# Kernel optimization log

Hardware: AMD Instinct MI355X
Metric: run time of the kernel (lower is better)

The kernel has to match this reference:

```python
import jax, jax.numpy as jnp
import numpy as np

N_NODES = 98304
N_GRAPHS = 2048
NODES_PER_GRAPH = 48
N_EDGES = 393216
NODE_IN = 128
EMB = 64
HID = 256
N_LAYERS = 6
ATTN_DIM = 256
N_HEADS = 4
HEAD_DIM = ATTN_DIM // N_HEADS
OUT_DIM = 1024


def setup_inputs() -> dict:
    key = jax.random.key(0)
    ks = iter(jax.random.split(key, 40))

    def nrm(shape, fan_in):
        return (jax.random.normal(next(ks), shape, dtype=jnp.float32)
                / np.float32(np.sqrt(fan_in)))

    x = jax.random.normal(next(ks), (N_NODES, NODE_IN), dtype=jnp.float32)
    edge_index = jax.random.randint(next(ks), (2, N_EDGES), 0, N_NODES, dtype=jnp.int32)
    batch = (jnp.arange(N_NODES, dtype=jnp.int32) // NODES_PER_GRAPH)

    inp = {
        "x": x,
        "edge_index": edge_index,
        "batch": batch,
        "W_embed": nrm((NODE_IN, EMB), NODE_IN),
        "b_embed": jnp.zeros((EMB,), jnp.float32),
        "W1": nrm((N_LAYERS, EMB, HID), EMB),
        "b1": jnp.zeros((N_LAYERS, HID), jnp.float32),
        "W2": nrm((N_LAYERS, HID, 2 * HID), HID),
        "b2": jnp.zeros((N_LAYERS, 2 * HID), jnp.float32),
        "W3": nrm((N_LAYERS, 2 * HID, EMB), 2 * HID),
        "b3": jnp.zeros((N_LAYERS, EMB), jnp.float32),
        "Wp": nrm((EMB, ATTN_DIM), EMB),
        "bp": jnp.zeros((ATTN_DIM,), jnp.float32),
        "q": jax.random.normal(next(ks), (1, ATTN_DIM), dtype=jnp.float32),
        "W_in": nrm((ATTN_DIM, 3 * ATTN_DIM), ATTN_DIM),
        "b_in": jnp.zeros((3 * ATTN_DIM,), jnp.float32),
        "W_out": nrm((ATTN_DIM, ATTN_DIM), ATTN_DIM),
        "b_out": jnp.zeros((ATTN_DIM,), jnp.float32),
        "Wh1": nrm((ATTN_DIM, HID), ATTN_DIM),
        "bh1": jnp.zeros((HID,), jnp.float32),
        "ln_g": jnp.ones((HID,), jnp.float32),
        "ln_b": jnp.zeros((HID,), jnp.float32),
        "Wh2": nrm((HID, OUT_DIM), HID),
        "bh2": jnp.zeros((OUT_DIM,), jnp.float32),
    }
    return inp


def _forward(x, edge_index, batch, W_embed, b_embed, W1, b1, W2, b2, W3, b3,
             Wp, bp, q, W_in, b_in, W_out, b_out, Wh1, bh1, ln_g, ln_b, Wh2, bh2):
    row = edge_index[0]  # only row is used, matching the torch module

    # node embed
    h = x @ W_embed + b_embed  # [N, 64]

    # 6 GNN layers: gather h[row] -> 3-layer MLP -> scatter_add back to row
    for l in range(N_LAYERS):
        m = jax.nn.relu(h[row] @ W1[l] + b1[l])          # [E, 256]
        m = jax.nn.relu(m @ W2[l] + b2[l])               # [E, 512]
        dh = m @ W3[l] + b3[l]                           # [E, 64]
        h = h + jax.ops.segment_sum(dh, row, num_segments=N_NODES)

    # attention pooling per graph (single learned query, 4 heads)
    hp = h @ Wp + bp                                     # [N, 256]
    Wq, Wk, Wv = W_in[:, :ATTN_DIM], W_in[:, ATTN_DIM:2 * ATTN_DIM], W_in[:, 2 * ATTN_DIM:]
    bq, bk, bv = b_in[:ATTN_DIM], b_in[ATTN_DIM:2 * ATTN_DIM], b_in[2 * ATTN_DIM:]

    qh = ((q @ Wq + bq).reshape(N_HEADS, HEAD_DIM)
          / jnp.asarray(np.sqrt(HEAD_DIM), jnp.float32))  # [H, D]
    k = (hp @ Wk + bk).reshape(N_NODES, N_HEADS, HEAD_DIM)
    v = (hp @ Wv + bv).reshape(N_NODES, N_HEADS, HEAD_DIM)

    scores = jnp.einsum('nhd,hd->nh', k, qh)             # [N, H]
    smax = jax.ops.segment_max(scores, batch, num_segments=N_GRAPHS)  # [B, H]
    e = jnp.exp(scores - smax[batch])
    denom = jax.ops.segment_sum(e, batch, num_segments=N_GRAPHS)      # [B, H]
    w = e / denom[batch]                                  # [N, H]
    pooled = jax.ops.segment_sum(w[:, :, None] * v, batch, num_segments=N_GRAPHS)  # [B, H, D]
    attn = pooled.reshape(N_GRAPHS, ATTN_DIM) @ W_out + b_out  # [B, 256]

    # projection head: ReLU -> Linear -> ReLU -> LayerNorm -> Linear
    t = jax.nn.relu(attn) @ Wh1 + bh1
    t = jax.nn.relu(t)
    mu = jnp.mean(t, axis=-1, keepdims=True)
    var = jnp.mean((t - mu) ** 2, axis=-1, keepdims=True)
    t = (t - mu) * jax.lax.rsqrt(var + 1e-5) * ln_g + ln_b
    return t @ Wh2 + bh2                                  # [B, 1024]


def reference(x, edge_index, batch, W_embed, b_embed, W1, b1, W2, b2, W3, b3,
              Wp, bp, q, W_in, b_in, W_out, b_out, Wh1, bh1, ln_g, ln_b, Wh2, bh2):
    return _forward(x, edge_index, batch, W_embed, b_embed, W1, b1, W2, b2, W3, b3,
                    Wp, bp, q, W_in, b_in, W_out, b_out, Wh1, bh1, ln_g, ln_b, Wh2, bh2)
```

## Files before the change

kernel.cpp:

```cpp
#include <hip/hip_runtime.h>
#include <hip/hip_bf16.h>

#define N_NODES 98304
#define N_GRAPHS 2048
#define N_EDGES 393216
#define EMB 64
#define HID 256
#define N_LAYERS_ 6

typedef __attribute__((ext_vector_type(8))) short short8v;
typedef __attribute__((ext_vector_type(4))) float f32x4;
#define MFMA16(a, b, c) __builtin_amdgcn_mfma_f32_16x16x32_bf16(a, b, c, 0, 0, 0)

__device__ __forceinline__ unsigned short f2bf(float x) {
    unsigned int u = __float_as_uint(x);
    u = (u + 0x7fffu + ((u >> 16) & 1u)) >> 16;
    return (unsigned short)u;
}
__device__ __forceinline__ float bf2f(unsigned short h) {
    return __uint_as_float(((unsigned int)h) << 16);
}
__device__ __forceinline__ int swz(int row, int col, int rowc) {
    return (row * rowc + col) ^ ((row & 7) << 3);
}

__global__ __launch_bounds__(256) void zero_cnt_kernel(int* __restrict__ cnt) {
    int i = blockIdx.x * 256 + threadIdx.x;
    if (i < N_NODES) cnt[i] = 0;
}
__global__ __launch_bounds__(256) void hist_kernel(const int* __restrict__ row,
                                                   int* __restrict__ cnt) {
    int i = blockIdx.x * 256 + threadIdx.x;
    if (i < N_EDGES) atomicAdd(&cnt[row[i]], 1);
}

__global__ __launch_bounds__(64) void prep_frag_kernel(
    const float* __restrict__ W, unsigned short* __restrict__ oh,
    unsigned short* __restrict__ ol, int K, int N)
{
    const int NF = N >> 4, KS = K >> 5;
    const int fpl = NF * KS;
    const int layer = blockIdx.x / fpl;
    const int fid = blockIdx.x % fpl;
    const int nf = fid / KS, ks = fid % KS;
    const int lane = threadIdx.x;
    const float* Wl = W + (size_t)layer * K * N;
    const int n = nf * 16 + (lane & 15);
    const int kb = ks * 32 + (lane >> 4) * 8;
    short8v vh, vl;
    #pragma unroll
    for (int j = 0; j < 8; j++) {
        float wv = Wl[(size_t)(kb + j) * N + n];
        unsigned short hi = f2bf(wv);
        vh[j] = (short)hi;
        vl[j] = (short)f2bf(wv - bf2f(hi));
    }
    size_t o = (size_t)layer * K * N + ((size_t)(nf * KS + ks) * 64 + lane) * 8;
    *reinterpret_cast<short8v*>(oh + o) = vh;
    *reinterpret_cast<short8v*>(ol + o) = vl;
}

__global__ __launch_bounds__(256) void gbuild_kernel(
    const float* __restrict__ Wp, const float* __restrict__ bp,
    const float* __restrict__ W_in, const float* __restrict__ b_in,
    float* __restrict__ Gm, float* __restrict__ Gd)
{
    const int idx = blockIdx.x * 256 + threadIdx.x;
    const int q = idx >> 8, p = idx & 255;
    float s = 0.f;
    if ((q >> 6) == (p >> 6)) {
        const float* wr = Wp + (q & 63) * 256;
        for (int j = 0; j < 256; j++) s += wr[j] * W_in[j * 768 + 512 + p];
    }
    Gm[q * 256 + p] = s;
    if (blockIdx.x == 0) {
        const int pp = threadIdx.x;
        float dsum = b_in[512 + pp];
        for (int j = 0; j < 256; j++) dsum += bp[j] * W_in[j * 768 + 512 + pp];
        Gd[pp] = dsum;
    }
}

__global__ __launch_bounds__(256) void embed_mfma_kernel(
    const float* __restrict__ x,
    const unsigned short* __restrict__ Weh, const unsigned short* __restrict__ Wel,
    const float* __restrict__ b, float* __restrict__ h)
{
    __shared__ __attribute__((aligned(16))) unsigned short xh[32 * 128];
    __shared__ __attribute__((aligned(16))) unsigned short xl[32 * 128];
    const int tid = threadIdx.x;
    const int lane = tid & 63, w = tid >> 6;
    const int lm = lane & 15, lq = lane >> 4;
    const int base = blockIdx.x * 32;
    {
        int row = tid >> 3, c0 = (tid & 7) * 16;
        const float4* p = reinterpret_cast<const float4*>(x + (size_t)(base + row) * 128 + c0);
        float4 u0 = p[0], u1 = p[1], u2 = p[2], u3 = p[3];
        float vals[16] = {u0.x,u0.y,u0.z,u0.w, u1.x,u1.y,u1.z,u1.w,
                          u2.x,u2.y,u2.z,u2.w, u3.x,u3.y,u3.z,u3.w};
        short8v vh0, vl0, vh1, vl1;
        #pragma unroll
        for (int j = 0; j < 8; j++) {
            unsigned short hi = f2bf(vals[j]);
            vh0[j] = (short)hi; vl0[j] = (short)f2bf(vals[j] - bf2f(hi));
            unsigned short hi1 = f2bf(vals[8 + j]);
            vh1[j] = (short)hi1; vl1[j] = (short)f2bf(vals[8 + j] - bf2f(hi1));
        }
        *reinterpret_cast<short8v*>(&xh[swz(row, c0, 128)]) = vh0;
        *reinterpret_cast<short8v*>(&xl[swz(row, c0, 128)]) = vl0;
        *reinterpret_cast<short8v*>(&xh[swz(row, c0 + 8, 128)]) = vh1;
        *reinterpret_cast<short8v*>(&xl[swz(row, c0 + 8, 128)]) = vl1;
    }
    __syncthreads();
    f32x4 acc0, acc1;
    {
        float bv = b[w * 16 + lm];
        acc0 = f32x4{bv, bv, bv, bv};
        acc1 = acc0;
    }
    #pragma unroll
    for (int ks = 0; ks < 4; ks++) {
        short8v a0h = *reinterpret_cast<const short8v*>(&xh[swz(lm, ks * 32 + lq * 8, 128)]);
        short8v a0l = *reinterpret_cast<const short8v*>(&xl[swz(lm, ks * 32 + lq * 8, 128)]);
        short8v a1h = *reinterpret_cast<const short8v*>(&xh[swz(16 + lm, ks * 32 + lq * 8, 128)]);
        short8v a1l = *reinterpret_cast<const short8v*>(&xl[swz(16 + lm, ks * 32 + lq * 8, 128)]);
        size_t bi = ((size_t)(w * 4 + ks) * 64 + lane) * 8;
        short8v bh = *reinterpret_cast<const short8v*>(Weh + bi);
        short8v bl = *reinterpret_cast<const short8v*>(Wel + bi);
        acc0 = MFMA16(a0h, bh, acc0); acc0 = MFMA16(a0l, bh, acc0); acc0 = MFMA16(a0h, bl, acc0);
        acc1 = MFMA16(a1h, bh, acc1); acc1 = MFMA16(a1l, bh, acc1); acc1 = MFMA16(a1h, bl, acc1);
    }
    #pragma unroll
    for (int r = 0; r < 4; r++) {
        h[(size_t)(base + lq * 4 + r) * 64 + w * 16 + lm] = acc0[r];
        h[(size_t)(base + 16 + lq * 4 + r) * 64 + w * 16 + lm] = acc1[r];
    }
}

__global__ __launch_bounds__(512, 4) void layer_mfma_kernel(
    float* __restrict__ h, const int* __restrict__ cnt,
    const unsigned short* __restrict__ W1h, const unsigned short* __restrict__ W1l,
    const float* __restrict__ b1,
    const unsigned short* __restrict__ W2h, const unsigned short* __restrict__ W2l,
    const float* __restrict__ b2,
    const unsigned short* __restrict__ W3h, const unsigned short* __restrict__ W3l,
    const float* __restrict__ b3)
{
    __shared__ __attribute__((aligned(16))) unsigned short hsh[32 * 64];
    __shared__ __attribute__((aligned(16))) unsigned short hsl[32 * 64];
    __shared__ __attribute__((aligned(16))) unsigned short m1h_[32 * 256];
    __shared__ __attribute__((aligned(16))) unsigned short m1l_[32 * 256];
    __shared__ __attribute__((aligned(16))) unsigned short m2h_[32 * 256];
    __shared__ __attribute__((aligned(16))) unsigned short m2l_[32 * 256];
    const int tid = threadIdx.x;
    const int lane = tid & 63, w = tid >> 6;
    const int lm = lane & 15, lq = lane >> 4;
    const int base = blockIdx.x * 32;

    {
        int row = tid >> 4, c0 = (tid & 15) * 4;
        const float4 u = *reinterpret_cast<const float4*>(h + (size_t)(base + row) * 64 + c0);
        float vals[4] = {u.x, u.y, u.z, u.w};
        unsigned short vh[4], vl[4];
        #pragma unroll
        for (int j = 0; j < 4; j++) {
            vh[j] = f2bf(vals[j]);
            vl[j] = f2bf(vals[j] - bf2f(vh[j]));
        }
        int idx = swz(row, c0, 64);
        *reinterpret_cast<uint2*>(&hsh[idx]) = *reinterpret_cast<uint2*>(vh);
        *reinterpret_cast<uint2*>(&hsl[idx]) = *reinterpret_cast<uint2*>(vl);
    }
    __syncthreads();

    {
        f32x4 acc[2][2];
        #pragma unroll
        for (int f = 0; f < 2; f++) {
            float bv = b1[(2 * w + f) * 16 + lm];
            acc[f][0] = f32x4{bv, bv, bv, bv};
            acc[f][1] = acc[f][0];
        }
        #pragma unroll
        for (int ks = 0; ks < 2; ks++) {
            short8v ah0 = *reinterpret_cast<const short8v*>(&hsh[swz(lm, ks * 32 + lq * 8, 64)]);
            short8v al0 = *reinterpret_cast<const short8v*>(&hsl[swz(lm, ks * 32 + lq * 8, 64)]);
            short8v ah1 = *reinterpret_cast<const short8v*>(&hsh[swz(16 + lm, ks * 32 + lq * 8, 64)]);
            short8v al1 = *reinterpret_cast<const short8v*>(&hsl[swz(16 + lm, ks * 32 + lq * 8, 64)]);
            #pragma unroll
            for (int f = 0; f < 2; f++) {
                size_t bi = ((size_t)((2 * w + f) * 2 + ks) * 64 + lane) * 8;
                short8v bh = *reinterpret_cast<const short8v*>(W1h + bi);
                short8v bl = *reinterpret_cast<const short8v*>(W1l + bi);
                acc[f][0] = MFMA16(ah0, bh, acc[f][0]);
                acc[f][0] = MFMA16(al0, bh, acc[f][0]);
                acc[f][0] = MFMA16(ah0, bl, acc[f][0]);
                acc[f][1] = MFMA16(ah1, bh, acc[f][1]);
                acc[f][1] = MFMA16(al1, bh, acc[f][1]);
                acc[f][1] = MFMA16(ah1, bl, acc[f][1]);
            }
        }
        #pragma unroll
        for (int f = 0; f < 2; f++)
            #pragma unroll
            for (int m = 0; m < 2; m++)
                #pragma unroll
                for (int r = 0; r < 4; r++) {
                    int row = m * 16 + lq * 4 + r;
                    int col = (2 * w + f) * 16 + lm;
                    float v = fmaxf(acc[f][m][r], 0.f);
                    unsigned short hi = f2bf(v);
                    m1h_[swz(row, col, 256)] = hi;
                    m1l_[swz(row, col, 256)] = f2bf(v - bf2f(hi));
                }
    }
    __syncthreads();

    const int nfc = w & 3, kq = w >> 2;
    f32x4 dacc[2];
    if (kq == 0) {
        float bv = b3[nfc * 16 + lm];
        dacc[0] = f32x4{bv, bv, bv, bv};
    } else {
        dacc[0] = f32x4{0.f, 0.f, 0.f, 0.f};
    }
    dacc[1] = dacc[0];

    #pragma unroll
    for (int c = 0; c < 2; ++c) {
        {
            f32x4 acc[2][2];
            #pragma unroll
            for (int f = 0; f < 2; f++) {
                float bv = b2[(c * 16 + 2 * w + f) * 16 + lm];
                acc[f][0] = f32x4{bv, bv, bv, bv};
                acc[f][1] = acc[f][0];
            }
            #pragma unroll
            for (int ks = 0; ks < 8; ks++) {
                short8v ah0 = *reinterpret_cast<const short8v*>(&m1h_[swz(lm, ks * 32 + lq * 8, 256)]);
                short8v al0 = *reinterpret_cast<const short8v*>(&m1l_[swz(lm, ks * 32 + lq * 8, 256)]);
                short8v ah1 = *reinterpret_cast<const short8v*>(&m1h_[swz(16 + lm, ks * 32 + lq * 8, 256)]);
                short8v al1 = *reinterpret_cast<const short8v*>(&m1l_[swz(16 + lm, ks * 32 + lq * 8, 256)]);
                #pragma unroll
                for (int f = 0; f < 2; f++) {
                    size_t bi = ((size_t)((c * 16 + 2 * w + f) * 8 + ks) * 64 + lane) * 8;
                    short8v bh = *reinterpret_cast<const short8v*>(W2h + bi);
                    short8v bl = *reinterpret_cast<const short8v*>(W2l + bi);
                    acc[f][0] = MFMA16(ah0, bh, acc[f][0]);
                    acc[f][0] = MFMA16(al0, bh, acc[f][0]);
                    acc[f][0] = MFMA16(ah0, bl, acc[f][0]);
                    acc[f][1] = MFMA16(ah1, bh, acc[f][1]);
                    acc[f][1] = MFMA16(al1, bh, acc[f][1]);
                    acc[f][1] = MFMA16(ah1, bl, acc[f][1]);
                }
            }
            #pragma unroll
            for (int f = 0; f < 2; f++)
                #pragma unroll
                for (int m = 0; m < 2; m++)
                    #pragma unroll
                    for (int r = 0; r < 4; r++) {
                        int row = m * 16 + lq * 4 + r;
                        int col = (2 * w + f) * 16 + lm;
                        float v = fmaxf(acc[f][m][r], 0.f);
                        unsigned short hi = f2bf(v);
                        m2h_[swz(row, col, 256)] = hi;
                        m2l_[swz(row, col, 256)] = f2bf(v - bf2f(hi));
                    }
        }
        __syncthreads();
        {
            #pragma unroll
            for (int kl = 0; kl < 4; kl++) {
                int ksl = kq * 4 + kl;
                short8v ah0 = *reinterpret_cast<const short8v*>(&m2h_[swz(lm, ksl * 32 + lq * 8, 256)]);
                short8v al0 = *reinterpret_cast<const short8v*>(&m2l_[swz(lm, ksl * 32 + lq * 8, 256)]);
                short8v ah1 = *reinterpret_cast<const short8v*>(&m2h_[swz(16 + lm, ksl * 32 + lq * 8, 256)]);
                short8v al1 = *reinterpret_cast<const short8v*>(&m2l_[swz(16 + lm, ksl * 32 + lq * 8, 256)]);
                int ksg = c * 8 + ksl;
                size_t bi = ((size_t)(nfc * 16 + ksg) * 64 + lane) * 8;
                short8v bh = *reinterpret_cast<const short8v*>(W3h + bi);
                short8v bl = *reinterpret_cast<const short8v*>(W3l + bi);
                dacc[0] = MFMA16(ah0, bh, dacc[0]);
                dacc[0] = MFMA16(al0, bh, dacc[0]);
                dacc[0] = MFMA16(ah0, bl, dacc[0]);
                dacc[1] = MFMA16(ah1, bh, dacc[1]);
                dacc[1] = MFMA16(al1, bh, dacc[1]);
                dacc[1] = MFMA16(ah1, bl, dacc[1]);
            }
        }
        __syncthreads();
    }

    float* scr = reinterpret_cast<float*>(m1h_);
    if (kq == 1) {
        #pragma unroll
        for (int m = 0; m < 2; m++)
            #pragma unroll
            for (int r = 0; r < 4; r++)
                scr[(m * 16 + lq * 4 + r) * 64 + nfc * 16 + lm] = dacc[m][r];
    }
    __syncthreads();
    if (kq == 0) {
        #pragma unroll
        for (int m = 0; m < 2; m++)
            #pragma unroll
            for (int r = 0; r < 4; r++) {
                int rr = base + m * 16 + lq * 4 + r;
                float dv = dacc[m][r] + scr[(m * 16 + lq * 4 + r) * 64 + nfc * 16 + lm];
                size_t gi = (size_t)rr * 64 + nfc * 16 + lm;
                h[gi] = h[gi] + (float)cnt[rr] * dv;
            }
    }
}

__global__ __launch_bounds__(256) void prec_kernel(
    const float* __restrict__ q, const float* __restrict__ W_in,
    const float* __restrict__ b_in, const float* __restrict__ Wp,
    const float* __restrict__ bp, float* __restrict__ prec)
{
    __shared__ float qh_s[256];
    __shared__ float u_s[4 * 256];
    const int tid = threadIdx.x;
    {
        float acc = b_in[tid];
        for (int j = 0; j < 256; j++) acc += q[j] * W_in[j * 768 + tid];
        qh_s[tid] = acc * 0.125f;
    }
    __syncthreads();
    {
        #pragma unroll
        for (int hd = 0; hd < 4; hd++) {
            float a = 0.f;
            for (int d = 0; d < 64; d++)
                a += W_in[tid * 768 + 256 + hd * 64 + d] * qh_s[hd * 64 + d];
            u_s[hd * 256 + tid] = a;
        }
    }
    __syncthreads();
    {
        int hd = tid >> 6, i = tid & 63;
        float a = 0.f;
        for (int j = 0; j < 256; j++) a += Wp[i * 256 + j] * u_s[hd * 256 + j];
        prec[hd * 64 + i] = a;
    }
    if (tid < 4) {
        float a = 0.f;
        for (int j = 0; j < 256; j++) a += bp[j] * u_s[tid * 256 + j];
        for (int d = 0; d < 64; d++) a += b_in[256 + tid * 64 + d] * qh_s[tid * 64 + d];
        prec[256 + tid] = a;
    }
}

__global__ __launch_bounds__(64) void attnpool_kernel(
    const float* __restrict__ h, const float* __restrict__ prec,
    float* __restrict__ hw)
{
    __shared__ float hs[48 * 65];
    __shared__ float ss[4 * 64];
    __shared__ float ds_[4];
    __shared__ float wl[48 * 4];
    const int lane = threadIdx.x;
    const int g = blockIdx.x;
    #pragma unroll
    for (int hd = 0; hd < 4; hd++) ss[hd * 64 + lane] = prec[hd * 64 + lane];
    if (lane < 4) ds_[lane] = prec[256 + lane];
    for (int r = 0; r < 48; r++)
        hs[r * 65 + lane] = h[((size_t)g * 48 + r) * 64 + lane];
    __syncthreads();
    float sc[4] = {0.f, 0.f, 0.f, 0.f};
    if (lane < 48) {
        #pragma unroll
        for (int hd = 0; hd < 4; hd++) sc[hd] = ds_[hd];
        for (int c = 0; c < 64; c++) {
            float a = hs[lane * 65 + c];
            #pragma unroll
            for (int hd = 0; hd < 4; hd++) sc[hd] += a * ss[hd * 64 + c];
        }
    }
    #pragma unroll
    for (int hd = 0; hd < 4; hd++) {
        float v = (lane < 48) ? sc[hd] : -3.0e38f;
        #pragma unroll
        for (int m = 32; m >= 1; m >>= 1) v = fmaxf(v, __shfl_xor(v, m, 64));
        float e = (lane < 48) ? __expf(sc[hd] - v) : 0.f;
        float s = e;
        #pragma unroll
        for (int m = 32; m >= 1; m >>= 1) s += __shfl_xor(s, m, 64);
        if (lane < 48) wl[lane * 4 + hd] = e / s;
    }
    __syncthreads();
    float acc[4] = {0.f, 0.f, 0.f, 0.f};
    for (int n = 0; n < 48; n++) {
        float hv = hs[n * 65 + lane];
        #pragma unroll
        for (int hd = 0; hd < 4; hd++) acc[hd] += wl[n * 4 + hd] * hv;
    }
    #pragma unroll
    for (int hd = 0; hd < 4; hd++) hw[(size_t)g * 256 + hd * 64 + lane] = acc[hd];
}

__device__ __forceinline__ void tail_stage(
    const unsigned short* __restrict__ inh, const unsigned short* __restrict__ inl,
    const unsigned short* __restrict__ wh, const unsigned short* __restrict__ wl,
    const float* __restrict__ bias, const bool do_relu,
    unsigned short* __restrict__ oth, unsigned short* __restrict__ otl,
    float* __restrict__ tf32,
    const int w, const int lane, const int lm, const int lq)
{
    f32x4 acc[2][2];
    #pragma unroll
    for (int f = 0; f < 2; f++) {
        float bv = bias[(2 * w + f) * 16 + lm];
        acc[f][0] = f32x4{bv, bv, bv, bv};
        acc[f][1] = acc[f][0];
    }
    #pragma unroll
    for (int ks = 0; ks < 8; ks++) {
        short8v ah0 = *reinterpret_cast<const short8v*>(&inh[swz(lm, ks * 32 + lq * 8, 256)]);
        short8v al0 = *reinterpret_cast<const short8v*>(&inl[swz(lm, ks * 32 + lq * 8, 256)]);
        short8v ah1 = *reinterpret_cast<const short8v*>(&inh[swz(16 + lm, ks * 32 + lq * 8, 256)]);
        short8v al1 = *reinterpret_cast<const short8v*>(&inl[swz(16 + lm, ks * 32 + lq * 8, 256)]);
        #pragma unroll
        for (int f = 0; f < 2; f++) {
            size_t bi = ((size_t)((2 * w + f) * 8 + ks) * 64 + lane) * 8;
            short8v bh = *reinterpret_cast<const short8v*>(wh + bi);
            short8v bl = *reinterpret_cast<const short8v*>(wl + bi);
            acc[f][0] = MFMA16(ah0, bh, acc[f][0]);
            acc[f][0] = MFMA16(al0, bh, acc[f][0]);
            acc[f][0] = MFMA16(ah0, bl, acc[f][0]);
            acc[f][1] = MFMA16(ah1, bh, acc[f][1]);
            acc[f][1] = MFMA16(al1, bh, acc[f][1]);
            acc[f][1] = MFMA16(ah1, bl, acc[f][1]);
        }
    }
    #pragma unroll
    for (int f = 0; f < 2; f++)
        #pragma unroll
        for (int m = 0; m < 2; m++)
            #pragma unroll
            for (int r = 0; r < 4; r++) {
                int row = m * 16 + lq * 4 + r;
                int col = (2 * w + f) * 16 + lm;
                float v = acc[f][m][r];
                if (do_relu) v = fmaxf(v, 0.f);
                if (tf32) {
                    tf32[row * 256 + col] = v;
                } else {
                    unsigned short hi = f2bf(v);
                    oth[swz(row, col, 256)] = hi;
                    otl[swz(row, col, 256)] = f2bf(v - bf2f(hi));
                }
            }
}

__global__ __launch_bounds__(512, 4) void tail_mfma_kernel(
    const float* __restrict__ hw,
    const unsigned short* __restrict__ Gh, const unsigned short* __restrict__ Gl,
    const float* __restrict__ Gd,
    const unsigned short* __restrict__ Woh, const unsigned short* __restrict__ Wol,
    const float* __restrict__ b_out,
    const unsigned short* __restrict__ Wh1h, const unsigned short* __restrict__ Wh1l,
    const float* __restrict__ bh1,
    const float* __restrict__ ln_g, const float* __restrict__ ln_b,
    const unsigned short* __restrict__ Wh2h, const unsigned short* __restrict__ Wh2l,
    const float* __restrict__ bh2,
    float* __restrict__ out)
{
    __shared__ __attribute__((aligned(16))) unsigned short L[32768];
    unsigned short* Ah = L;
    unsigned short* Al = L + 8192;
    unsigned short* Bh = L + 16384;
    unsigned short* Bl = L + 24576;
    float* tf = reinterpret_cast<float*>(L + 16384);
    const int tid = threadIdx.x;
    const int lane = tid & 63, w = tid >> 6;
    const int lm = lane & 15, lq = lane >> 4;
    const int g0 = blockIdx.x * 32;

    {
        const float4* hp = reinterpret_cast<const float4*>(hw + (size_t)g0 * 256);
        #pragma unroll
        for (int i = 0; i < 4; i++) {
            int e = tid + 512 * i;
            int row = e >> 6, c0 = (e & 63) * 4;
            float4 u = hp[e];
            float vals[4] = {u.x, u.y, u.z, u.w};
            unsigned short vh[4], vl[4];
            #pragma unroll
            for (int j = 0; j < 4; j++) {
                vh[j] = f2bf(vals[j]);
                vl[j] = f2bf(vals[j] - bf2f(vh[j]));
            }
            int idx = swz(row, c0, 256);
            *reinterpret_cast<uint2*>(&Ah[idx]) = *reinterpret_cast<uint2*>(vh);
            *reinterpret_cast<uint2*>(&Al[idx]) = *reinterpret_cast<uint2*>(vl);
        }
    }
    __syncthreads();
    tail_stage(Ah, Al, Gh, Gl, Gd, false, Bh, Bl, nullptr, w, lane, lm, lq);
    __syncthreads();
    tail_stage(Bh, Bl, Woh, Wol, b_out, true, Ah, Al, nullptr, w, lane, lm, lq);
    __syncthreads();
    tail_stage(Ah, Al, Wh1h, Wh1l, bh1, true, nullptr, nullptr, tf, w, lane, lm, lq);
    __syncthreads();
    {
        const int row = tid >> 4, l16 = tid & 15;
        float s = 0.f;
        #pragma unroll
        for (int k = 0; k < 16; k++) s += tf[row * 256 + l16 + 16 * k];
        #pragma unroll
        for (int m = 1; m < 16; m <<= 1) s += __shfl_xor(s, m, 16);
        float mu = s * (1.f / 256.f);
        float v = 0.f;
        #pragma unroll
        for (int k = 0; k < 16; k++) {
            float d = tf[row * 256 + l16 + 16 * k] - mu;
            v += d * d;
        }
        #pragma unroll
        for (int m = 1; m < 16; m <<= 1) v += __shfl_xor(v, m, 16);
        float rs = rsqrtf(v * (1.f / 256.f) + 1e-5f);
        #pragma unroll
        for (int k = 0; k < 16; k++) {
            int col = l16 + 16 * k;
            float val = (tf[row * 256 + col] - mu) * rs * ln_g[col] + ln_b[col];
            unsigned short hi = f2bf(val);
            int idx = swz(row, col, 256);
            Ah[idx] = hi;
            Al[idx] = f2bf(val - bf2f(hi));
        }
    }
    __syncthreads();
    {
        f32x4 acc[8][2];
        #pragma unroll
        for (int f = 0; f < 8; f++) {
            float bv = bh2[(8 * w + f) * 16 + lm];
            acc[f][0] = f32x4{bv, bv, bv, bv};
            acc[f][1] = acc[f][0];
        }
        #pragma unroll
        for (int ks = 0; ks < 8; ks++) {
            short8v ah0 = *reinterpret_cast<const short8v*>(&Ah[swz(lm, ks * 32 + lq * 8, 256)]);
            short8v al0 = *reinterpret_cast<const short8v*>(&Al[swz(lm, ks * 32 + lq * 8, 256)]);
            short8v ah1 = *reinterpret_cast<const short8v*>(&Ah[swz(16 + lm, ks * 32 + lq * 8, 256)]);
            short8v al1 = *reinterpret_cast<const short8v*>(&Al[swz(16 + lm, ks * 32 + lq * 8, 256)]);
            #pragma unroll
            for (int f = 0; f < 8; f++) {
                size_t bi = ((size_t)((8 * w + f) * 8 + ks) * 64 + lane) * 8;
                short8v bh = *reinterpret_cast<const short8v*>(Wh2h + bi);
                short8v bl = *reinterpret_cast<const short8v*>(Wh2l + bi);
                acc[f][0] = MFMA16(ah0, bh, acc[f][0]);
                acc[f][0] = MFMA16(al0, bh, acc[f][0]);
                acc[f][0] = MFMA16(ah0, bl, acc[f][0]);
                acc[f][1] = MFMA16(ah1, bh, acc[f][1]);
                acc[f][1] = MFMA16(al1, bh, acc[f][1]);
                acc[f][1] = MFMA16(ah1, bl, acc[f][1]);
            }
        }
        #pragma unroll
        for (int f = 0; f < 8; f++)
            #pragma unroll
            for (int m = 0; m < 2; m++)
                #pragma unroll
                for (int r = 0; r < 4; r++)
                    out[(size_t)(g0 + m * 16 + lq * 4 + r) * 1024 + (8 * w + f) * 16 + lm]
                        = acc[f][m][r];
    }
}

extern "C" void kernel_launch(void* const* d_in, const int* in_sizes, int n_in,
                              void* d_out, int out_size, void* d_ws, size_t ws_size,
                              hipStream_t stream) {
    const float* x       = (const float*)d_in[0];
    const int*   edge    = (const int*)d_in[1];
    const float* W_embed = (const float*)d_in[3];
    const float* b_embed = (const float*)d_in[4];
    const float* W1 = (const float*)d_in[5];
    const float* b1 = (const float*)d_in[6];
    const float* W2 = (const float*)d_in[7];
    const float* b2 = (const float*)d_in[8];
    const float* W3 = (const float*)d_in[9];
    const float* b3 = (const float*)d_in[10];
    const float* Wp = (const float*)d_in[11];
    const float* bp = (const float*)d_in[12];
    const float* q  = (const float*)d_in[13];
    const float* W_in  = (const float*)d_in[14];
    const float* b_in  = (const float*)d_in[15];
    const float* W_out = (const float*)d_in[16];
    const float* b_out = (const float*)d_in[17];
    const float* Wh1 = (const float*)d_in[18];
    const float* bh1 = (const float*)d_in[19];
    const float* ln_g = (const float*)d_in[20];
    const float* ln_b = (const float*)d_in[21];
    const float* Wh2 = (const float*)d_in[22];
    const float* bh2 = (const float*)d_in[23];
    float* out = (float*)d_out;

    char* ws = (char*)d_ws;
    int*   cnt  = (int*)(ws + 0);
    float* h    = (float*)(ws + 393216);
    float* hw   = (float*)(ws + 25559040);
    float* prec = (float*)(ws + 27656192);
    unsigned short* W1h = (unsigned short*)(ws + 27657232);
    unsigned short* W1l = (unsigned short*)(ws + 27853840);
    unsigned short* W2h = (unsigned short*)(ws + 28050448);
    unsigned short* W2l = (unsigned short*)(ws + 29623312);
    unsigned short* W3h = (unsigned short*)(ws + 31196176);
    unsigned short* W3l = (unsigned short*)(ws + 31589392);
    unsigned short* Weh = (unsigned short*)(ws + 31982608);
    unsigned short* Wel = (unsigned short*)(ws + 31998992);
    float* Gm  = (float*)(ws + 32015376);
    float* Gd  = (float*)(ws + 32277520);
    unsigned short* Gfh  = (unsigned short*)(ws + 32278544);
    unsigned short* Gfl  = (unsigned short*)(ws + 32409616);
    unsigned short* Wofh = (unsigned short*)(ws + 32540688);
    unsigned short* Wofl = (unsigned short*)(ws + 32671760);
    unsigned short* Wh1fh= (unsigned short*)(ws + 32802832);
    unsigned short* Wh1fl= (unsigned short*)(ws + 32933904);
    unsigned short* Wh2fh= (unsigned short*)(ws + 33064976);
    unsigned short* Wh2fl= (unsigned short*)(ws + 33589264);

    zero_cnt_kernel<<<N_NODES / 256, 256, 0, stream>>>(cnt);
    hist_kernel<<<N_EDGES / 256, 256, 0, stream>>>(edge, cnt);

    prep_frag_kernel<<<1 * (64 / 16) * (128 / 32), 64, 0, stream>>>(W_embed, Weh, Wel, 128, 64);
    prep_frag_kernel<<<6 * (256 / 16) * (64 / 32), 64, 0, stream>>>(W1, W1h, W1l, 64, 256);
    prep_frag_kernel<<<6 * (512 / 16) * (256 / 32), 64, 0, stream>>>(W2, W2h, W2l, 256, 512);
    prep_frag_kernel<<<6 * (64 / 16) * (512 / 32), 64, 0, stream>>>(W3, W3h, W3l, 512, 64);

    gbuild_kernel<<<256, 256, 0, stream>>>(Wp, bp, W_in, b_in, Gm, Gd);
    prep_frag_kernel<<<(256 / 16) * (256 / 32), 64, 0, stream>>>(Gm, Gfh, Gfl, 256, 256);
    prep_frag_kernel<<<(256 / 16) * (256 / 32), 64, 0, stream>>>(W_out, Wofh, Wofl, 256, 256);
    prep_frag_kernel<<<(256 / 16) * (256 / 32), 64, 0, stream>>>(Wh1, Wh1fh, Wh1fl, 256, 256);
    prep_frag_kernel<<<(1024 / 16) * (256 / 32), 64, 0, stream>>>(Wh2, Wh2fh, Wh2fl, 256, 1024);

    embed_mfma_kernel<<<N_NODES / 32, 256, 0, stream>>>(x, Weh, Wel, b_embed, h);
    for (int l = 0; l < N_LAYERS_; l++) {
        layer_mfma_kernel<<<N_NODES / 32, 512, 0, stream>>>(
            h, cnt,
            W1h + (size_t)l * EMB * HID,     W1l + (size_t)l * EMB * HID,     b1 + (size_t)l * HID,
            W2h + (size_t)l * HID * 2 * HID, W2l + (size_t)l * HID * 2 * HID, b2 + (size_t)l * 2 * HID,
            W3h + (size_t)l * 2 * HID * EMB, W3l + (size_t)l * 2 * HID * EMB, b3 + (size_t)l * EMB);
    }
    prec_kernel<<<1, 256, 0, stream>>>(q, W_in, b_in, Wp, bp, prec);
    attnpool_kernel<<<N_GRAPHS, 64, 0, stream>>>(h, prec, hw);
    tail_mfma_kernel<<<N_GRAPHS / 32, 512, 0, stream>>>(
        hw, Gfh, Gfl, Gd, Wofh, Wofl, b_out, Wh1fh, Wh1fl, bh1,
        ln_g, ln_b, Wh2fh, Wh2fl, bh2, out);
}
```

Baseline: 882.2 us.

## Use hardware packed bf16 conversion and shrink layer kernel LDS for higher occupancy

Replaces the software round-to-nearest bf16 split with the v_cvt_pk_bf16_f32 instruction in all hi/lo conversion paths, cutting the ALU work of the split-bf16 packing. The layer kernel's MLP second stage now processes 128-column chunks in four passes instead of 256 in two, which halves the m2 buffer and lets it alias the input buffer. That lowers LDS use so launch bounds can go from 4 to 6 blocks per CU. The costs are more barriers and more chunk passes, tighter register limits, and scattered 16-bit LDS stores in store_quad.

Measured after the change: 877.5 us. About the same (-0.5%).

```diff
diff --git a/kernel.cpp b/kernel.cpp
--- a/kernel.cpp
+++ b/kernel.cpp
@@ -19,6 +19,11 @@
 }
 __device__ __forceinline__ float bf2f(unsigned short h) {
     return __uint_as_float(((unsigned int)h) << 16);
+}
+__device__ __forceinline__ unsigned int cvtpk(float a, float b) {
+    unsigned int r;
+    asm("v_cvt_pk_bf16_f32 %0, %1, %2" : "=v"(r) : "v"(a), "v"(b));
+    return r;
 }
 __device__ __forceinline__ int swz(int row, int col, int rowc) {
     return (row * rowc + col) ^ ((row & 7) << 3);
@@ -95,21 +100,19 @@
     {
         int row = tid >> 3, c0 = (tid & 7) * 16;
         const float4* p = reinterpret_cast<const float4*>(x + (size_t)(base + row) * 128 + c0);
-        float4 u0 = p[0], u1 = p[1], u2 = p[2], u3 = p[3];
-        float vals[16] = {u0.x,u0.y,u0.z,u0.w, u1.x,u1.y,u1.z,u1.w,
-                          u2.x,u2.y,u2.z,u2.w, u3.x,u3.y,u3.z,u3.w};
-        short8v vh0, vl0, vh1, vl1;
-        #pragma unroll
-        for (int j = 0; j < 8; j++) {
-            unsigned short hi = f2bf(vals[j]);
-            vh0[j] = (short)hi; vl0[j] = (short)f2bf(vals[j] - bf2f(hi));
-            unsigned short hi1 = f2bf(vals[8 + j]);
-            vh1[j] = (short)hi1; vl1[j] = (short)f2bf(vals[8 + j] - bf2f(hi1));
-        }
-        *reinterpret_cast<short8v*>(&xh[swz(row, c0, 128)]) = vh0;
-        *reinterpret_cast<short8v*>(&xl[swz(row, c0, 128)]) = vl0;
-        *reinterpret_cast<short8v*>(&xh[swz(row, c0 + 8, 128)]) = vh1;
-        *reinterpret_cast<short8v*>(&xl[swz(row, c0 + 8, 128)]) = vl1;
+        #pragma unroll
+        for (int g = 0; g < 4; g++) {
+            float4 u = p[g];
+            unsigned int p01 = cvtpk(u.x, u.y);
+            unsigned int p23 = cvtpk(u.z, u.w);
+            float h0 = __uint_as_float(p01 << 16), h1 = __uint_as_float(p01 & 0xffff0000u);
+            float h2 = __uint_as_float(p23 << 16), h3 = __uint_as_float(p23 & 0xffff0000u);
+            unsigned int q01 = cvtpk(u.x - h0, u.y - h1);
+            unsigned int q23 = cvtpk(u.z - h2, u.w - h3);
+            int idx = swz(row, c0 + g * 4, 128);
+            *reinterpret_cast<uint2*>(&xh[idx]) = make_uint2(p01, p23);
+            *reinterpret_cast<uint2*>(&xl[idx]) = make_uint2(q01, q23);
+        }
     }
     __syncthreads();
     f32x4 acc0, acc1;
@@ -137,7 +140,28 @@
     }
 }
 
-__global__ __launch_bounds__(512, 4) void layer_mfma_kernel(
+__device__ __forceinline__ void store_quad(
+    unsigned short* __restrict__ oh, unsigned short* __restrict__ ol,
+    float v0, float v1, float v2, float v3,
+    int row0, int col, int rowc)
+{
+    unsigned int p01 = cvtpk(v0, v1);
+    unsigned int p23 = cvtpk(v2, v3);
+    float h0 = __uint_as_float(p01 << 16), h1 = __uint_as_float(p01 & 0xffff0000u);
+    float h2 = __uint_as_float(p23 << 16), h3 = __uint_as_float(p23 & 0xffff0000u);
+    unsigned int q01 = cvtpk(v0 - h0, v1 - h1);
+    unsigned int q23 = cvtpk(v2 - h2, v3 - h3);
+    oh[swz(row0 + 0, col, rowc)] = (unsigned short)p01;
+    oh[swz(row0 + 1, col, rowc)] = (unsigned short)(p01 >> 16);
+    oh[swz(row0 + 2, col, rowc)] = (unsigned short)p23;
+    oh[swz(row0 + 3, col, rowc)] = (unsigned short)(p23 >> 16);
+    ol[swz(row0 + 0, col, rowc)] = (unsigned short)q01;
+    ol[swz(row0 + 1, col, rowc)] = (unsigned short)(q01 >> 16);
+    ol[swz(row0 + 2, col, rowc)] = (unsigned short)q23;
+    ol[swz(row0 + 3, col, rowc)] = (unsigned short)(q23 >> 16);
+}
+
+__global__ __launch_bounds__(512, 6) void layer_mfma_kernel(
     float* __restrict__ h, const int* __restrict__ cnt,
     const unsigned short* __restrict__ W1h, const unsigned short* __restrict__ W1l,
     const float* __restrict__ b1,
@@ -146,12 +170,13 @@
     const unsigned short* __restrict__ W3h, const unsigned short* __restrict__ W3l,
     const float* __restrict__ b3)
 {
-    __shared__ __attribute__((aligned(16))) unsigned short hsh[32 * 64];
-    __shared__ __attribute__((aligned(16))) unsigned short hsl[32 * 64];
-    __shared__ __attribute__((aligned(16))) unsigned short m1h_[32 * 256];
-    __shared__ __attribute__((aligned(16))) unsigned short m1l_[32 * 256];
-    __shared__ __attribute__((aligned(16))) unsigned short m2h_[32 * 256];
-    __shared__ __attribute__((aligned(16))) unsigned short m2l_[32 * 256];
+    __shared__ __attribute__((aligned(16))) unsigned short R0[4096];
+    __shared__ __attribute__((aligned(16))) unsigned short m1h_[8192];
+    __shared__ __attribute__((aligned(16))) unsigned short m1l_[8192];
+    __shared__ __attribute__((aligned(16))) unsigned short m2l_[4096];
+    unsigned short* hsh = R0;
+    unsigned short* hsl = R0 + 2048;
+    unsigned short* m2h_ = R0;
     const int tid = threadIdx.x;
     const int lane = tid & 63, w = tid >> 6;
     const int lm = lane & 15, lq = lane >> 4;
@@ -160,16 +185,15 @@
     {
         int row = tid >> 4, c0 = (tid & 15) * 4;
         const float4 u = *reinterpret_cast<const float4*>(h + (size_t)(base + row) * 64 + c0);
-        float vals[4] = {u.x, u.y, u.z, u.w};
-        unsigned short vh[4], vl[4];
-        #pragma unroll
-        for (int j = 0; j < 4; j++) {
-            vh[j] = f2bf(vals[j]);
-            vl[j] = f2bf(vals[j] - bf2f(vh[j]));
-        }
+        unsigned int p01 = cvtpk(u.x, u.y);
+        unsigned int p23 = cvtpk(u.z, u.w);
+        float h0 = __uint_as_float(p01 << 16), h1 = __uint_as_float(p01 & 0xffff0000u);
+        float h2 = __uint_as_float(p23 << 16), h3 = __uint_as_float(p23 & 0xffff0000u);
+        unsigned int q01 = cvtpk(u.x - h0, u.y - h1);
+        unsigned int q23 = cvtpk(u.z - h2, u.w - h3);
         int idx = swz(row, c0, 64);
-        *reinterpret_cast<uint2*>(&hsh[idx]) = *reinterpret_cast<uint2*>(vh);
-        *reinterpret_cast<uint2*>(&hsl[idx]) = *reinterpret_cast<uint2*>(vl);
+        *reinterpret_cast<uint2*>(&hsh[idx]) = make_uint2(p01, p23);
+        *reinterpret_cast<uint2*>(&hsl[idx]) = make_uint2(q01, q23);
     }
     __syncthreads();
 
@@ -204,15 +228,10 @@
         for (int f = 0; f < 2; f++)
             #pragma unroll
             for (int m = 0; m < 2; m++)
-                #pragma unroll
-                for (int r = 0; r < 4; r++) {
-                    int row = m * 16 + lq * 4 + r;
-                    int col = (2 * w + f) * 16 + lm;
-                    float v = fmaxf(acc[f][m][r], 0.f);
-                    unsigned short hi = f2bf(v);
-                    m1h_[swz(row, col, 256)] = hi;
-                    m1l_[swz(row, col, 256)] = f2bf(v - bf2f(hi));
-                }
+                store_quad(m1h_, m1l_,
+                           fmaxf(acc[f][m][0], 0.f), fmaxf(acc[f][m][1], 0.f),
+                           fmaxf(acc[f][m][2], 0.f), fmaxf(acc[f][m][3], 0.f),
+                           m * 16 + lq * 4, (2 * w + f) * 16 + lm, 256);
     }
     __syncthreads();
 
@@ -227,14 +246,14 @@
     dacc[1] = dacc[0];
 
     #pragma unroll
-    for (int c = 0; c < 2; ++c) {
+    for (int c = 0; c < 4; ++c) {
         {
-            f32x4 acc[2][2];
-            #pragma unroll
-            for (int f = 0; f < 2; f++) {
-                float bv = b2[(c * 16 + 2 * w + f) * 16 + lm];
-                acc[f][0] = f32x4{bv, bv, bv, bv};
-                acc[f][1] = acc[f][0];
+            const int nfg = c * 8 + w;
+            f32x4 acc[2];
+            {
+                float bv = b2[nfg * 16 + lm];
+                acc[0] = f32x4{bv, bv, bv, bv};
+                acc[1] = acc[0];
             }
             #pragma unroll
             for (int ks = 0; ks < 8; ks++) {
@@ -242,43 +261,33 @@
                 short8v al0 = *reinterpret_cast<const short8v*>(&m1l_[swz(lm, ks * 32 + lq * 8, 256)]);
                 short8v ah1 = *reinterpret_cast<const short8v*>(&m1h_[swz(16 + lm, ks * 32 + lq * 8, 256)]);
                 short8v al1 = *reinterpret_cast<const short8v*>(&m1l_[swz(16 + lm, ks * 32 + lq * 8, 256)]);
-                #pragma unroll
-                for (int f = 0; f < 2; f++) {
-                    size_t bi = ((size_t)((c * 16 + 2 * w + f) * 8 + ks) * 64 + lane) * 8;
-                    short8v bh = *reinterpret_cast<const short8v*>(W2h + bi);
-                    short8v bl = *reinterpret_cast<const short8v*>(W2l + bi);
-                    acc[f][0] = MFMA16(ah0, bh, acc[f][0]);
-                    acc[f][0] = MFMA16(al0, bh, acc[f][0]);
-                    acc[f][0] = MFMA16(ah0, bl, acc[f][0]);
-                    acc[f][1] = MFMA16(ah1, bh, acc[f][1]);
-                    acc[f][1] = MFMA16(al1, bh, acc[f][1]);
-                    acc[f][1] = MFMA16(ah1, bl, acc[f][1]);
-                }
+                size_t bi = ((size_t)(nfg * 8 + ks) * 64 + lane) * 8;
+                short8v bh = *reinterpret_cast<const short8v*>(W2h + bi);
+                short8v bl = *reinterpret_cast<const short8v*>(W2l + bi);
+                acc[0] = MFMA16(ah0, bh, acc[0]);
+                acc[0] = MFMA16(al0, bh, acc[0]);
+                acc[0] = MFMA16(ah0, bl, acc[0]);
+                acc[1] = MFMA16(ah1, bh, acc[1]);
+                acc[1] = MFMA16(al1, bh, acc[1]);
+                acc[1] = MFMA16(ah1, bl, acc[1]);
             }
             #pragma unroll
-            for (int f = 0; f < 2; f++)
-                #pragma unroll
-                for (int m = 0; m < 2; m++)
-                    #pragma unroll
-                    for (int r = 0; r < 4; r++) {
-                        int row = m * 16 + lq * 4 + r;
-                        int col = (2 * w + f) * 16 + lm;
-                        float v = fmaxf(acc[f][m][r], 0.f);
-                        unsigned short hi = f2bf(v);
-                        m2h_[swz(row, col, 256)] = hi;
-                        m2l_[swz(row, col, 256)] = f2bf(v - bf2f(hi));
-                    }
+            for (int m = 0; m < 2; m++)
+                store_quad(m2h_, m2l_,
+                           fmaxf(acc[m][0], 0.f), fmaxf(acc[m][1], 0.f),
+                           fmaxf(acc[m][2], 0.f), fmaxf(acc[m][3], 0.f),
+                           m * 16 + lq * 4, w * 16 + lm, 128);
         }
         __syncthreads();
         {
             #pragma unroll
-            for (int kl = 0; kl < 4; kl++) {
-                int ksl = kq * 4 + kl;
-                short8v ah0 = *reinterpret_cast<const short8v*>(&m2h_[swz(lm, ksl * 32 + lq * 8, 256)]);
-                short8v al0 = *reinterpret_cast<const short8v*>(&m2l_[swz(lm, ksl * 32 + lq * 8, 256)]);
-                short8v ah1 = *reinterpret_cast<const short8v*>(&m2h_[swz(16 + lm, ksl * 32 + lq * 8, 256)]);
-                short8v al1 = *reinterpret_cast<const short8v*>(&m2l_[swz(16 + lm, ksl * 32 + lq * 8, 256)]);
-                int ksg = c * 8 + ksl;
+            for (int kl = 0; kl < 2; kl++) {
+                int ksl = kq * 2 + kl;
+                short8v ah0 = *reinterpret_cast<const short8v*>(&m2h_[swz(lm, ksl * 32 + lq * 8, 128)]);
+                short8v al0 = *reinterpret_cast<const short8v*>(&m2l_[swz(lm, ksl * 32 + lq * 8, 128)]);
+                short8v ah1 = *reinterpret_cast<const short8v*>(&m2h_[swz(16 + lm, ksl * 32 + lq * 8, 128)]);
+                short8v al1 = *reinterpret_cast<const short8v*>(&m2l_[swz(16 + lm, ksl * 32 + lq * 8, 128)]);
+                int ksg = c * 4 + ksl;
                 size_t bi = ((size_t)(nfc * 16 + ksg) * 64 + lane) * 8;
                 short8v bh = *reinterpret_cast<const short8v*>(W3h + bi);
                 short8v bl = *reinterpret_cast<const short8v*>(W3l + bi);
@@ -438,21 +447,24 @@
     #pragma unroll
     for (int f = 0; f < 2; f++)
         #pragma unroll
-        for (int m = 0; m < 2; m++)
-            #pragma unroll
-            for (int r = 0; r < 4; r++) {
-                int row = m * 16 + lq * 4 + r;
-                int col = (2 * w + f) * 16 + lm;
-                float v = acc[f][m][r];
-                if (do_relu) v = fmaxf(v, 0.f);
-                if (tf32) {
-                    tf32[row * 256 + col] = v;
-                } else {
-                    unsigned short hi = f2bf(v);
-                    oth[swz(row, col, 256)] = hi;
-                    otl[swz(row, col, 256)] = f2bf(v - bf2f(hi));
+        for (int m = 0; m < 2; m++) {
+            if (tf32) {
+                #pragma unroll
+                for (int r = 0; r < 4; r++) {
+                    float v = acc[f][m][r];
+                    if (do_relu) v = fmaxf(v, 0.f);
+                    tf32[(m * 16 + lq * 4 + r) * 256 + (2 * w + f) * 16 + lm] = v;
                 }
+            } else {
+                float v0 = acc[f][m][0], v1 = acc[f][m][1], v2 = acc[f][m][2], v3 = acc[f][m][3];
+                if (do_relu) {
+                    v0 = fmaxf(v0, 0.f); v1 = fmaxf(v1, 0.f);
+                    v2 = fmaxf(v2, 0.f); v3 = fmaxf(v3, 0.f);
+                }
+                store_quad(oth, otl, v0, v1, v2, v3,
+                           m * 16 + lq * 4, (2 * w + f) * 16 + lm, 256);
             }
+        }
 }
 
 __global__ __launch_bounds__(512, 4) void tail_mfma_kernel(
@@ -486,16 +498,15 @@
             int e = tid + 512 * i;
             int row = e >> 6, c0 = (e & 63) * 4;
             float4 u = hp[e];
-            float vals[4] = {u.x, u.y, u.z, u.w};
-            unsigned short vh[4], vl[4];
-            #pragma unroll
-            for (int j = 0; j < 4; j++) {
-                vh[j] = f2bf(vals[j]);
-                vl[j] = f2bf(vals[j] - bf2f(vh[j]));
-            }
+            unsigned int p01 = cvtpk(u.x, u.y);
+            unsigned int p23 = cvtpk(u.z, u.w);
+            float h0 = __uint_as_float(p01 << 16), h1 = __uint_as_float(p01 & 0xffff0000u);
+            float h2 = __uint_as_float(p23 << 16), h3 = __uint_as_float(p23 & 0xffff0000u);
+            unsigned int q01 = cvtpk(u.x - h0, u.y - h1);
+            unsigned int q23 = cvtpk(u.z - h2, u.w - h3);
             int idx = swz(row, c0, 256);
-            *reinterpret_cast<uint2*>(&Ah[idx]) = *reinterpret_cast<uint2*>(vh);
-            *reinterpret_cast<uint2*>(&Al[idx]) = *reinterpret_cast<uint2*>(vl);
+            *reinterpret_cast<uint2*>(&Ah[idx]) = make_uint2(p01, p23);
+            *reinterpret_cast<uint2*>(&Al[idx]) = make_uint2(q01, q23);
         }
     }
     __syncthreads();
```
